# Kernel optimization log

Hardware: AMD Instinct MI355X
Metric: run time of the kernel (lower is better)

The kernel has to match this reference:

```python
import jax, jax.numpy as jnp
import numpy as np
import math

B, S, H, NH = 1, 2048, 1024, 16  # batch, seq, hidden, heads


def setup_inputs() -> dict:
    key = jax.random.key(0)
    ks = jax.random.split(key, 12)
    inp = {
        "query": jax.random.normal(ks[0], (B, S, H), dtype=jnp.float32),
        "key": jax.random.normal(ks[1], (B, S, H), dtype=jnp.float32),
        "value": jax.random.normal(ks[2], (B, S, H), dtype=jnp.float32),
        "attention_mask": jax.random.randint(ks[3], (1, 1, S, S), 0, 2, dtype=jnp.int32),
        # torch nn.Linear params: y = x @ W.T + b, W init ~ U(-1/sqrt(H), 1/sqrt(H))
        "Wq": jax.random.uniform(ks[4], (H, H), jnp.float32, -1, 1) / math.sqrt(H),
        "bq": jax.random.uniform(ks[5], (H,), jnp.float32, -1, 1) / math.sqrt(H),
        "Wk": jax.random.uniform(ks[6], (H, H), jnp.float32, -1, 1) / math.sqrt(H),
        "bk": jax.random.uniform(ks[7], (H,), jnp.float32, -1, 1) / math.sqrt(H),
        "Wv": jax.random.uniform(ks[8], (H, H), jnp.float32, -1, 1) / math.sqrt(H),
        "bv": jax.random.uniform(ks[9], (H,), jnp.float32, -1, 1) / math.sqrt(H),
        "Wo": jax.random.uniform(ks[10], (H, H), jnp.float32, -1, 1) / math.sqrt(H),
        "bo": jax.random.uniform(ks[11], (H,), jnp.float32, -1, 1) / math.sqrt(H),
        "head": NH,
        "hidden_size": H,
    }
    return inp


def reference(query, key, value, attention_mask, Wq, bq, Wk, bk, Wv, bv, Wo, bo, head, hidden_size):
    b, s, _ = query.shape
    d_k = hidden_size // head

    def proj(x, W, bias):
        # [b, s, hidden] -> [b, head, s, d_k]
        y = x @ W.T + bias
        return y.reshape(b, s, head, d_k).transpose(0, 2, 1, 3)

    q = proj(query, Wq, bq)
    k = proj(key, Wk, bk)
    v = proj(value, Wv, bv)

    # naive full score matrix, as in the source (scale by sqrt(d_k) = last dim of q)
    scores = jnp.einsum("bhqd,bhkd->bhqk", q, k) / math.sqrt(d_k)
    # faithful quirk: masked positions are set to 0 (not -inf) before softmax
    scores = jnp.where(attention_mask == 0, jnp.zeros((), scores.dtype), scores)
    attn = jax.nn.softmax(scores, axis=-1)

    out = jnp.einsum("bhqk,bhkd->bhqd", attn, v)  # [b, head, s, d_k]
    out = out.transpose(0, 2, 1, 3).reshape(b, s, head * d_k)
    return out @ Wo.T + bo
```

## Files before the change

kernel.cpp:

```cpp
#include <hip/hip_runtime.h>
#include <hip/hip_bf16.h>


#define S_LEN 2048
#define HID   1024
#define NHEAD 16
#define DK    64

typedef unsigned short u16;
typedef __attribute__((ext_vector_type(8))) short bf16x8;
typedef __attribute__((ext_vector_type(4))) float f32x4;

#if defined(__has_builtin)
#if __has_builtin(__builtin_amdgcn_exp2f)
#define EXP2F(x) __builtin_amdgcn_exp2f(x)
#else
#define EXP2F(x) exp2f(x)
#endif
#else
#define EXP2F(x) exp2f(x)
#endif

__device__ __forceinline__ void load16_lds(const void* g, void* l) {
  __builtin_amdgcn_global_load_lds(
      (const __attribute__((address_space(1))) void*)g,
      (__attribute__((address_space(3))) void*)l, 16, 0, 0);
}

__device__ __forceinline__ short bfbits(float x) {
  __hip_bfloat16 h = __float2bfloat16(x);
  return *(short*)&h;
}
__device__ __forceinline__ bf16x8 cvt8(float4 a, float4 b) {
  bf16x8 r;
  r[0] = bfbits(a.x); r[1] = bfbits(a.y); r[2] = bfbits(a.z); r[3] = bfbits(a.w);
  r[4] = bfbits(b.x); r[5] = bfbits(b.y); r[6] = bfbits(b.z); r[7] = bfbits(b.w);
  return r;
}
__device__ __forceinline__ float bf2f(u16 u) {
  unsigned v = (unsigned)u << 16;
  return *(float*)&v;
}

__global__ __launch_bounds__(256) void cvtW_kernel(
    const float* __restrict__ wq, const float* __restrict__ wk,
    const float* __restrict__ wv, const float* __restrict__ wo,
    u16* __restrict__ Wbf) {
  const int y = blockIdx.y;
  const float* src = y == 0 ? wq : (y == 1 ? wk : (y == 2 ? wv : wo));
  size_t i = ((size_t)blockIdx.x * 256 + threadIdx.x) * 8;
  float4 a = *(const float4*)(src + i);
  float4 b = *(const float4*)(src + i + 4);
  *(bf16x8*)(Wbf + (size_t)y * (HID * HID) + i) = cvt8(a, b);
}

__global__ void pack_mask_kernel(const int* __restrict__ mask,
                                 unsigned int* __restrict__ bits) {
  int w = blockIdx.x * blockDim.x + threadIdx.x;
  const int4* p = (const int4*)(mask + (size_t)w * 32);
  unsigned word = 0;
#pragma unroll
  for (int i = 0; i < 8; ++i) {
    int4 v = p[i];
    word |= (unsigned)(v.x != 0) << (i * 4 + 0);
    word |= (unsigned)(v.y != 0) << (i * 4 + 1);
    word |= (unsigned)(v.z != 0) << (i * 4 + 2);
    word |= (unsigned)(v.w != 0) << (i * 4 + 3);
  }
  bits[w] = word;
}

__global__ __launch_bounds__(256) void gemm_qkv(
    const float* __restrict__ qf32, const float* __restrict__ kf32,
    const float* __restrict__ vf32, const u16* __restrict__ Wbf,
    const float* __restrict__ bq, const float* __restrict__ bk,
    const float* __restrict__ bv, u16* __restrict__ Qb,
    u16* __restrict__ Kb, u16* __restrict__ Vt) {
  constexpr int Mm = 2048, Nn = 1024, Kk = 1024, NIT = 16;
  const int z = blockIdx.z;
  const float* A = z == 0 ? qf32 : (z == 1 ? kf32 : vf32);
  const u16* W = Wbf + (size_t)z * (HID * HID);
  const float* bias = z == 0 ? bq : (z == 1 ? bk : bv);
  u16* C = z == 0 ? Qb : (z == 1 ? Kb : Vt);
  const float oscale = (z == 0) ? 0.125f * 1.4426950408889634f : 1.0f;
  const int transpose = (z == 2);

  const int tid = threadIdx.x, lane = tid & 63, wave = tid >> 6;
  const int q4 = lane >> 4, c16 = lane & 15;
  const int bx = blockIdx.x;
  const int mBase = (bx & 31) * 64;
  const int nBase = (bx >> 5) * 128;
  const int wn = wave * 32;

  __shared__ __align__(16) u16 As[2][2][64 * 32];
  __shared__ __align__(16) u16 Bs[2][2][128 * 32];

  f32x4 acc[4][2] = {};
  const int srow = lane >> 2, se8 = (lane & 3) * 8;

  auto issueW = [&](int it, int buf) {
#pragma unroll
    for (int j = 0; j < 4; ++j) {
      int u = wave * 4 + j, h = u >> 3, grp = u & 7;
      load16_lds(W + (size_t)(nBase + grp * 16 + srow) * Kk + it * 64 +
                     h * 32 + se8,
                 &Bs[buf][h][grp * 512]);
    }
  };
  float4 ar[2][2];
  auto loadA = [&](int it) {
#pragma unroll
    for (int j = 0; j < 2; ++j) {
      int u = wave * 2 + j, h = u >> 2, grp = u & 3;
      const float* s = A + (size_t)(mBase + grp * 16 + srow) * Kk + it * 64 +
                       h * 32 + se8;
      ar[j][0] = *(const float4*)s;
      ar[j][1] = *(const float4*)(s + 4);
    }
  };
  auto storeA = [&](int buf) {
#pragma unroll
    for (int j = 0; j < 2; ++j) {
      int u = wave * 2 + j, h = u >> 2, grp = u & 3;
      *(bf16x8*)&As[buf][h][grp * 512 + srow * 32 + se8] =
          cvt8(ar[j][0], ar[j][1]);
    }
  };

  loadA(0);
  storeA(0);
  issueW(0, 0);
  __syncthreads();

  for (int it = 0; it < NIT; ++it) {
    const int buf = it & 1, nbuf = buf ^ 1;
    if (it + 1 < NIT) {
      issueW(it + 1, nbuf);
      loadA(it + 1);
    }
#pragma unroll
    for (int kk = 0; kk < 2; ++kk) {
      bf16x8 af[4], bfr[2];
#pragma unroll
      for (int t = 0; t < 4; ++t)
        af[t] = *(const bf16x8*)&As[buf][kk][(t * 16 + c16) * 32 + q4 * 8];
#pragma unroll
      for (int t = 0; t < 2; ++t)
        bfr[t] = *(const bf16x8*)&Bs[buf][kk][(wn + t * 16 + c16) * 32 + q4 * 8];
#pragma unroll
      for (int mt = 0; mt < 4; ++mt)
#pragma unroll
        for (int nt = 0; nt < 2; ++nt)
          acc[mt][nt] = __builtin_amdgcn_mfma_f32_16x16x32_bf16(
              af[mt], bfr[nt], acc[mt][nt], 0, 0, 0);
    }
    if (it + 1 < NIT) storeA(nbuf);
    __syncthreads();
  }

#pragma unroll
  for (int nt = 0; nt < 2; ++nt) {
    int col = nBase + wn + nt * 16 + c16;
    float bv2 = bias[col];
#pragma unroll
    for (int mt = 0; mt < 4; ++mt) {
#pragma unroll
      for (int r = 0; r < 4; ++r) {
        int row = mBase + mt * 16 + q4 * 4 + r;
        float v = (acc[mt][nt][r] + bv2) * oscale;
        if (transpose)
          ((__hip_bfloat16*)C)[(size_t)col * Mm + row] = __float2bfloat16(v);
        else
          ((__hip_bfloat16*)C)[(size_t)row * Nn + col] = __float2bfloat16(v);
      }
    }
  }
}

__global__ __launch_bounds__(256) void attn_kernel(
    const u16* __restrict__ Qb, const u16* __restrict__ Kb,
    const u16* __restrict__ Vt, const unsigned* __restrict__ mbits,
    u16* __restrict__ partO, float* __restrict__ partL) {
  constexpr int NITA = S_LEN / 2 / 64;
  const int qt = blockIdx.x, h = blockIdx.y, zz = blockIdx.z;
  const int tid = threadIdx.x, lane = tid & 63, wave = tid >> 6;
  const int q4 = lane >> 4, c16 = lane & 15;

  __shared__ __align__(16) u16 Ks[2][2][64 * 32];
  __shared__ __align__(16) u16 Vs[2][2][64 * 32];
  __shared__ __align__(16) u16 Ps[4][2 * 16 * 72];

  const int wq0 = qt * 128 + wave * 32;

  bf16x8 qf[2][2];
#pragma unroll
  for (int t = 0; t < 2; ++t)
#pragma unroll
    for (int kk = 0; kk < 2; ++kk)
      qf[t][kk] = *(const bf16x8*)(Qb + (size_t)(wq0 + t * 16 + c16) * HID +
                                   h * DK + kk * 32 + q4 * 8);

  f32x4 o[2][4] = {};
  float l_lane[2][4] = {};

  const int srow = lane >> 2;
  const int se8  = (lane & 3) * 8;
  const int kvbase = zz * (S_LEN / 2);

  auto issueKV = [&](int it, int buf) {
    const int kv0 = kvbase + it * 64;
#pragma unroll
    for (int j = 0; j < 4; ++j) {
      int i = wave * 4 + j;
      if (i < 8) {
        int half = i >> 2, grp = i & 3;
        load16_lds(Kb + (size_t)(kv0 + grp * 16 + srow) * HID + h * DK +
                       half * 32 + se8,
                   &Ks[buf][half][grp * 512]);
      } else {
        int ii = i - 8;
        int half = ii >> 2, grp = ii & 3;
        load16_lds(Vt + (size_t)(h * DK + grp * 16 + srow) * S_LEN + kv0 +
                       half * 32 + se8,
                   &Vs[buf][half][grp * 512]);
      }
    }
  };

  issueKV(0, 0);
  __syncthreads();

  for (int it = 0; it < NITA; ++it) {
    const int buf = it & 1, nbuf = buf ^ 1;
    const int kv0 = kvbase + it * 64;
    if (it + 1 < NITA) issueKV(it + 1, nbuf);

    f32x4 sv[2][4];
#pragma unroll
    for (int nt = 0; nt < 4; ++nt) {
      bf16x8 kf0 = *(const bf16x8*)&Ks[buf][0][(nt * 16 + c16) * 32 + q4 * 8];
      bf16x8 kf1 = *(const bf16x8*)&Ks[buf][1][(nt * 16 + c16) * 32 + q4 * 8];
#pragma unroll
      for (int t = 0; t < 2; ++t) {
        f32x4 a = {};
        a = __builtin_amdgcn_mfma_f32_16x16x32_bf16(qf[t][0], kf0, a, 0, 0, 0);
        a = __builtin_amdgcn_mfma_f32_16x16x32_bf16(qf[t][1], kf1, a, 0, 0, 0);
        sv[t][nt] = a;
      }
    }

#pragma unroll
    for (int t = 0; t < 2; ++t)
#pragma unroll
      for (int r = 0; r < 4; ++r) {
        int row = wq0 + t * 16 + q4 * 4 + r;
        const unsigned* mrow = mbits + (size_t)row * 64 + (kv0 >> 5);
        unsigned w0 = mrow[0], w1 = mrow[1];
#pragma unroll
        for (int nt = 0; nt < 4; ++nt) {
          unsigned word = (nt < 2) ? w0 : w1;
          int bit = ((nt & 1) * 16) + c16;
          float s = ((word >> bit) & 1u) ? sv[t][nt][r] : 0.0f;
          float p = EXP2F(s);
          sv[t][nt][r] = p;
          l_lane[t][r] += p;
        }
      }

    u16* pw = &Ps[wave][0];
#pragma unroll
    for (int t = 0; t < 2; ++t)
#pragma unroll
      for (int r = 0; r < 4; ++r)
#pragma unroll
        for (int nt = 0; nt < 4; ++nt)
          ((__hip_bfloat16*)pw)[t * 1152 + (q4 * 4 + r) * 72 + nt * 16 + c16] =
              __float2bfloat16(sv[t][nt][r]);
    asm volatile("s_waitcnt lgkmcnt(0)" ::: "memory");

    bf16x8 vb[2][4];
#pragma unroll
    for (int kk = 0; kk < 2; ++kk)
#pragma unroll
      for (int nt = 0; nt < 4; ++nt)
        vb[kk][nt] =
            *(const bf16x8*)&Vs[buf][kk][(nt * 16 + c16) * 32 + q4 * 8];
#pragma unroll
    for (int t = 0; t < 2; ++t)
#pragma unroll
      for (int kk = 0; kk < 2; ++kk) {
        bf16x8 pa = *(const bf16x8*)&pw[t * 1152 + c16 * 72 + kk * 32 + q4 * 8];
#pragma unroll
        for (int nt = 0; nt < 4; ++nt)
          o[t][nt] = __builtin_amdgcn_mfma_f32_16x16x32_bf16(pa, vb[kk][nt],
                                                             o[t][nt], 0, 0, 0);
      }
    __syncthreads();
  }

#pragma unroll
  for (int t = 0; t < 2; ++t)
#pragma unroll
    for (int r = 0; r < 4; ++r) {
      float s = l_lane[t][r];
#pragma unroll
      for (int d = 1; d < 16; d <<= 1) s += __shfl_xor(s, d);
      l_lane[t][r] = s;
    }

#pragma unroll
  for (int t = 0; t < 2; ++t)
#pragma unroll
    for (int r = 0; r < 4; ++r) {
      int row = wq0 + t * 16 + q4 * 4 + r;
#pragma unroll
      for (int nt = 0; nt < 4; ++nt)
        ((__hip_bfloat16*)partO)[((size_t)zz * S_LEN + row) * HID + h * DK +
                                 nt * 16 + c16] = __float2bfloat16(o[t][nt][r]);
      if (c16 == 0)
        partL[((size_t)zz * NHEAD + h) * S_LEN + row] = l_lane[t][r];
    }
}

__global__ __launch_bounds__(256) void gemm_out(
    const u16* __restrict__ partO, const float* __restrict__ partL,
    const u16* __restrict__ Wo, const float* __restrict__ bo,
    float* __restrict__ out) {
  constexpr int Nn = 1024, Kk = 1024, NIT = 16;
  constexpr size_t M2 = (size_t)S_LEN * HID;
  const int tid = threadIdx.x, lane = tid & 63, wave = tid >> 6;
  const int q4 = lane >> 4, c16 = lane & 15;
  const int bx = blockIdx.x;
  const int mBase = (bx & 63) * 32;
  const int nBase = (bx >> 6) * 128;
  const int wn = wave * 32;

  __shared__ __align__(16) u16 As[2][2][32 * 32];
  __shared__ __align__(16) u16 Bs[2][2][128 * 32];

  f32x4 acc[2][2] = {};
  const int srow = lane >> 2, se8 = (lane & 3) * 8;

  auto issueW = [&](int it, int buf) {
#pragma unroll
    for (int j = 0; j < 4; ++j) {
      int u = wave * 4 + j, h = u >> 3, grp = u & 7;
      load16_lds(Wo + (size_t)(nBase + grp * 16 + srow) * Kk + it * 64 +
                     h * 32 + se8,
                 &Bs[buf][h][grp * 512]);
    }
  };
  bf16x8 a0r, a1r;
  float invr;
  auto loadA = [&](int it) {
    int u = wave, h = u >> 1, grp = u & 1;
    int row = mBase + grp * 16 + srow;
    size_t off = (size_t)row * Kk + it * 64 + h * 32 + se8;
    a0r = *(const bf16x8*)(partO + off);
    a1r = *(const bf16x8*)(partO + M2 + off);
    float l = partL[(size_t)it * S_LEN + row] +
              partL[((size_t)NHEAD + it) * S_LEN + row];
    invr = 1.0f / l;
  };
  auto storeA = [&](int buf) {
    int u = wave, h = u >> 1, grp = u & 1;
    bf16x8 r;
#pragma unroll
    for (int j = 0; j < 8; ++j)
      r[j] = bfbits((bf2f((u16)a0r[j]) + bf2f((u16)a1r[j])) * invr);
    *(bf16x8*)&As[buf][h][grp * 512 + srow * 32 + se8] = r;
  };

  loadA(0);
  storeA(0);
  issueW(0, 0);
  __syncthreads();

  for (int it = 0; it < NIT; ++it) {
    const int buf = it & 1, nbuf = buf ^ 1;
    if (it + 1 < NIT) {
      issueW(it + 1, nbuf);
      loadA(it + 1);
    }
#pragma unroll
    for (int kk = 0; kk < 2; ++kk) {
      bf16x8 af[2], bfr[2];
#pragma unroll
      for (int t = 0; t < 2; ++t)
        af[t] = *(const bf16x8*)&As[buf][kk][(t * 16 + c16) * 32 + q4 * 8];
#pragma unroll
      for (int t = 0; t < 2; ++t)
        bfr[t] = *(const bf16x8*)&Bs[buf][kk][(wn + t * 16 + c16) * 32 + q4 * 8];
#pragma unroll
      for (int mt = 0; mt < 2; ++mt)
#pragma unroll
        for (int nt = 0; nt < 2; ++nt)
          acc[mt][nt] = __builtin_amdgcn_mfma_f32_16x16x32_bf16(
              af[mt], bfr[nt], acc[mt][nt], 0, 0, 0);
    }
    if (it + 1 < NIT) storeA(nbuf);
    __syncthreads();
  }

#pragma unroll
  for (int nt = 0; nt < 2; ++nt) {
    int col = nBase + wn + nt * 16 + c16;
    float bv = bo[col];
#pragma unroll
    for (int mt = 0; mt < 2; ++mt)
#pragma unroll
      for (int r = 0; r < 4; ++r) {
        int row = mBase + mt * 16 + q4 * 4 + r;
        out[(size_t)row * Nn + col] = acc[mt][nt][r] + bv;
      }
  }
}

extern "C" void kernel_launch(void* const* d_in, const int* in_sizes, int n_in,
                              void* d_out, int out_size, void* d_ws, size_t ws_size,
                              hipStream_t stream) {
  const float* q    = (const float*)d_in[0];
  const float* k    = (const float*)d_in[1];
  const float* v    = (const float*)d_in[2];
  const int*   mask = (const int*)d_in[3];
  const float* Wq = (const float*)d_in[4];
  const float* bq = (const float*)d_in[5];
  const float* Wk = (const float*)d_in[6];
  const float* bk = (const float*)d_in[7];
  const float* Wv = (const float*)d_in[8];
  const float* bv = (const float*)d_in[9];
  const float* Wo = (const float*)d_in[10];
  const float* bo = (const float*)d_in[11];

  const size_t M2 = (size_t)S_LEN * HID;
  const size_t W1 = (size_t)HID * HID;
  const size_t need = (4 * W1 + 2 * M2 + 3 * M2) * 2 +
                      (size_t)S_LEN * 64 * 4 + 2 * NHEAD * S_LEN * 4;
  if (ws_size < need) return;

  u16* Wbf = (u16*)d_ws;
  u16* partO = Wbf + 4 * W1;
  u16* Qb = partO + 2 * M2;
  u16* Kb = Qb + M2;
  u16* Vt = Kb + M2;
  unsigned* mbits = (unsigned*)(Vt + M2);
  float* partL = (float*)(mbits + (size_t)S_LEN * 64);

  hipLaunchKernelGGL(cvtW_kernel, dim3(512, 4), dim3(256), 0, stream,
                     Wq, Wk, Wv, Wo, Wbf);

  hipLaunchKernelGGL(pack_mask_kernel, dim3((S_LEN * (S_LEN / 32)) / 256),
                     dim3(256), 0, stream, mask, mbits);

  hipLaunchKernelGGL(gemm_qkv, dim3(256, 1, 3), dim3(256), 0, stream,
                     q, k, v, Wbf, bq, bk, bv, Qb, Kb, Vt);

  hipLaunchKernelGGL(attn_kernel, dim3(S_LEN / 128, NHEAD, 2), dim3(256), 0,
                     stream, Qb, Kb, Vt, mbits, partO, partL);

  hipLaunchKernelGGL(gemm_out, dim3(512), dim3(256), 0, stream,
                     partO, partL, Wbf + 3 * W1, bo, (float*)d_out);
}
```

Before: 206.0 us.

## Merge weight-convert and mask-pack kernels; split attention KV into four chunks

Folds weight bf16 conversion and mask bit-packing into one prep launch, removing a kernel launch. Makes the attention key split count a runtime parameter and raises it from two to four when workspace permits, giving 1024 attention blocks instead of 512 for better CU occupancy. The output GEMM now sums a variable number of partial outputs and row sums. This adds partial-output traffic and reads in gemm_out, and a runtime loop over splits there.

```diff
diff --git a/kernel.cpp b/kernel.cpp
--- a/kernel.cpp
+++ b/kernel.cpp
@@ -42,32 +42,32 @@
   return *(float*)&v;
 }
 
-__global__ __launch_bounds__(256) void cvtW_kernel(
+__global__ __launch_bounds__(256) void prep_kernel(
     const float* __restrict__ wq, const float* __restrict__ wk,
     const float* __restrict__ wv, const float* __restrict__ wo,
-    u16* __restrict__ Wbf) {
+    const int* __restrict__ mask, u16* __restrict__ Wbf,
+    unsigned int* __restrict__ bits) {
   const int y = blockIdx.y;
-  const float* src = y == 0 ? wq : (y == 1 ? wk : (y == 2 ? wv : wo));
-  size_t i = ((size_t)blockIdx.x * 256 + threadIdx.x) * 8;
-  float4 a = *(const float4*)(src + i);
-  float4 b = *(const float4*)(src + i + 4);
-  *(bf16x8*)(Wbf + (size_t)y * (HID * HID) + i) = cvt8(a, b);
-}
-
-__global__ void pack_mask_kernel(const int* __restrict__ mask,
-                                 unsigned int* __restrict__ bits) {
-  int w = blockIdx.x * blockDim.x + threadIdx.x;
-  const int4* p = (const int4*)(mask + (size_t)w * 32);
-  unsigned word = 0;
-#pragma unroll
-  for (int i = 0; i < 8; ++i) {
-    int4 v = p[i];
-    word |= (unsigned)(v.x != 0) << (i * 4 + 0);
-    word |= (unsigned)(v.y != 0) << (i * 4 + 1);
-    word |= (unsigned)(v.z != 0) << (i * 4 + 2);
-    word |= (unsigned)(v.w != 0) << (i * 4 + 3);
-  }
-  bits[w] = word;
+  if (y < 4) {
+    const float* src = y == 0 ? wq : (y == 1 ? wk : (y == 2 ? wv : wo));
+    size_t i = ((size_t)blockIdx.x * 256 + threadIdx.x) * 8;
+    float4 a = *(const float4*)(src + i);
+    float4 b = *(const float4*)(src + i + 4);
+    *(bf16x8*)(Wbf + (size_t)y * (HID * HID) + i) = cvt8(a, b);
+  } else {
+    int w = blockIdx.x * 256 + threadIdx.x;
+    const int4* p = (const int4*)(mask + (size_t)w * 32);
+    unsigned word = 0;
+#pragma unroll
+    for (int i = 0; i < 8; ++i) {
+      int4 v = p[i];
+      word |= (unsigned)(v.x != 0) << (i * 4 + 0);
+      word |= (unsigned)(v.y != 0) << (i * 4 + 1);
+      word |= (unsigned)(v.z != 0) << (i * 4 + 2);
+      word |= (unsigned)(v.w != 0) << (i * 4 + 3);
+    }
+    bits[w] = word;
+  }
 }
 
 __global__ __launch_bounds__(256) void gemm_qkv(
@@ -181,8 +181,8 @@
     const u16* __restrict__ Qb, const u16* __restrict__ Kb,
     const u16* __restrict__ Vt, const unsigned* __restrict__ mbits,
     u16* __restrict__ partO, float* __restrict__ partL) {
-  constexpr int NITA = S_LEN / 2 / 64;
   const int qt = blockIdx.x, h = blockIdx.y, zz = blockIdx.z;
+  const int nita = (S_LEN / 64) / gridDim.z;
   const int tid = threadIdx.x, lane = tid & 63, wave = tid >> 6;
   const int q4 = lane >> 4, c16 = lane & 15;
 
@@ -205,7 +205,7 @@
 
   const int srow = lane >> 2;
   const int se8  = (lane & 3) * 8;
-  const int kvbase = zz * (S_LEN / 2);
+  const int kvbase = zz * nita * 64;
 
   auto issueKV = [&](int it, int buf) {
     const int kv0 = kvbase + it * 64;
@@ -230,10 +230,10 @@
   issueKV(0, 0);
   __syncthreads();
 
-  for (int it = 0; it < NITA; ++it) {
+  for (int it = 0; it < nita; ++it) {
     const int buf = it & 1, nbuf = buf ^ 1;
     const int kv0 = kvbase + it * 64;
-    if (it + 1 < NITA) issueKV(it + 1, nbuf);
+    if (it + 1 < nita) issueKV(it + 1, nbuf);
 
     f32x4 sv[2][4];
 #pragma unroll
@@ -325,7 +325,7 @@
 __global__ __launch_bounds__(256) void gemm_out(
     const u16* __restrict__ partO, const float* __restrict__ partL,
     const u16* __restrict__ Wo, const float* __restrict__ bo,
-    float* __restrict__ out) {
+    float* __restrict__ out, int nsplit) {
   constexpr int Nn = 1024, Kk = 1024, NIT = 16;
   constexpr size_t M2 = (size_t)S_LEN * HID;
   const int tid = threadIdx.x, lane = tid & 63, wave = tid >> 6;
@@ -350,24 +350,28 @@
                  &Bs[buf][h][grp * 512]);
     }
   };
-  bf16x8 a0r, a1r;
+  bf16x8 asr[4];
   float invr;
   auto loadA = [&](int it) {
     int u = wave, h = u >> 1, grp = u & 1;
     int row = mBase + grp * 16 + srow;
     size_t off = (size_t)row * Kk + it * 64 + h * 32 + se8;
-    a0r = *(const bf16x8*)(partO + off);
-    a1r = *(const bf16x8*)(partO + M2 + off);
-    float l = partL[(size_t)it * S_LEN + row] +
-              partL[((size_t)NHEAD + it) * S_LEN + row];
+    float l = 0.f;
+    for (int s = 0; s < nsplit; ++s) {
+      asr[s] = *(const bf16x8*)(partO + (size_t)s * M2 + off);
+      l += partL[((size_t)s * NHEAD + it) * S_LEN + row];
+    }
     invr = 1.0f / l;
   };
   auto storeA = [&](int buf) {
     int u = wave, h = u >> 1, grp = u & 1;
     bf16x8 r;
 #pragma unroll
-    for (int j = 0; j < 8; ++j)
-      r[j] = bfbits((bf2f((u16)a0r[j]) + bf2f((u16)a1r[j])) * invr);
+    for (int j = 0; j < 8; ++j) {
+      float v = bf2f((u16)asr[0][j]);
+      for (int s = 1; s < nsplit; ++s) v += bf2f((u16)asr[s][j]);
+      r[j] = bfbits(v * invr);
+    }
     *(bf16x8*)&As[buf][h][grp * 512 + srow * 32 + se8] = r;
   };
 
@@ -434,30 +438,31 @@
 
   const size_t M2 = (size_t)S_LEN * HID;
   const size_t W1 = (size_t)HID * HID;
-  const size_t need = (4 * W1 + 2 * M2 + 3 * M2) * 2 +
-                      (size_t)S_LEN * 64 * 4 + 2 * NHEAD * S_LEN * 4;
-  if (ws_size < need) return;
+
+  auto need_for = [&](int ns) {
+    return (4 * W1 + (size_t)ns * M2 + 3 * M2) * 2 +
+           (size_t)S_LEN * 64 * 4 + (size_t)ns * NHEAD * S_LEN * 4;
+  };
+  int nsplit = (ws_size >= need_for(4)) ? 4 : 2;
+  if (ws_size < need_for(2)) return;
 
   u16* Wbf = (u16*)d_ws;
   u16* partO = Wbf + 4 * W1;
-  u16* Qb = partO + 2 * M2;
+  u16* Qb = partO + (size_t)nsplit * M2;
   u16* Kb = Qb + M2;
   u16* Vt = Kb + M2;
   unsigned* mbits = (unsigned*)(Vt + M2);
   float* partL = (float*)(mbits + (size_t)S_LEN * 64);
 
-  hipLaunchKernelGGL(cvtW_kernel, dim3(512, 4), dim3(256), 0, stream,
-                     Wq, Wk, Wv, Wo, Wbf);
-
-  hipLaunchKernelGGL(pack_mask_kernel, dim3((S_LEN * (S_LEN / 32)) / 256),
-                     dim3(256), 0, stream, mask, mbits);
+  hipLaunchKernelGGL(prep_kernel, dim3(512, 5), dim3(256), 0, stream,
+                     Wq, Wk, Wv, Wo, mask, Wbf, mbits);
 
   hipLaunchKernelGGL(gemm_qkv, dim3(256, 1, 3), dim3(256), 0, stream,
                      q, k, v, Wbf, bq, bk, bv, Qb, Kb, Vt);
 
-  hipLaunchKernelGGL(attn_kernel, dim3(S_LEN / 128, NHEAD, 2), dim3(256), 0,
-                     stream, Qb, Kb, Vt, mbits, partO, partL);
+  hipLaunchKernelGGL(attn_kernel, dim3(S_LEN / 128, NHEAD, nsplit), dim3(256),
+                     0, stream, Qb, Kb, Vt, mbits, partO, partL);
 
   hipLaunchKernelGGL(gemm_out, dim3(512), dim3(256), 0, stream,
-                     partO, partL, Wbf + 3 * W1, bo, (float*)d_out);
-}
+                     partO, partL, Wbf + 3 * W1, bo, (float*)d_out, nsplit);
+}
```

Measured after the change: 595.2 us. 2.89x slower.
